# Performance work log

Hardware: AMD Instinct MI355X
Metric: run time of the kernel (lower is better)

Reference implementation:

```python
import jax, jax.numpy as jnp
import numpy as np

K = 8          # max_output_degree (complete 8-ary tree)
DEPTH = 7      # number of levels
LEVEL_OFFS = [(K**l - 1) // (K - 1) for l in range(DEPTH + 1)]  # [0,1,9,73,...]
N = LEVEL_OFFS[DEPTH]  # 299593 nodes
V, X, H, O = 32000, 128, 128, 128


def setup_inputs() -> dict:
    key = jax.random.key(0)
    ks = jax.random.split(key, 7)
    x = jax.random.randint(ks[0], (N,), 0, V, dtype=jnp.int32)
    mask = jnp.ones((N,), dtype=jnp.int32)
    # children of node i are K*i+1 .. K*i+K; out-of-range -> sentinel N (zero pad row)
    ch = np.arange(N, dtype=np.int64)[:, None] * K + 1 + np.arange(K, dtype=np.int64)[None, :]
    children = jnp.asarray(np.where(ch < N, ch, N).astype(np.int32))
    s = 0.02
    emb = jax.random.normal(ks[1], (V, X), dtype=jnp.float32) * s
    W_in = jax.random.normal(ks[2], (X, H), dtype=jnp.float32) * s
    b_in = jnp.zeros((H,), dtype=jnp.float32)
    U = jax.random.normal(ks[3], (H, H), dtype=jnp.float32) * s
    W_out = jax.random.normal(ks[4], (H, O), dtype=jnp.float32) * s
    b_out = jnp.zeros((O,), dtype=jnp.float32)
    return {"x": x, "mask": mask, "children": children, "emb": emb,
            "W_in": W_in, "b_in": b_in, "U": U, "W_out": W_out, "b_out": b_out}


def reference(x, mask, children, emb, W_in, b_in, U, b_out=None, W_out=None, **_):
    # keyword-safe wrapper not used; real signature below
    raise NotImplementedError


def reference(x, mask, children, emb, W_in, b_in, U, W_out, b_out):
    mf = mask.astype(jnp.float32)[:, None]                 # [N,1]
    embeds = emb[x * mask]                                 # [N,X] input_module(x*mask)
    h_input = (embeds @ W_in + b_in) * mf                  # [N,H] W_in(embeds)*mask
    h = jnp.zeros((N + 1, h_input.shape[1]), dtype=h_input.dtype)  # row N = zero pad
    # bottom-up topological propagation, level by level
    for l in range(DEPTH - 1, -1, -1):
        s, e = LEVEL_OFFS[l], LEVEL_OFFS[l + 1]
        if l == DEPTH - 1:
            # leaves: no children messages
            h_new = jnp.tanh(h_input[s:e])
        else:
            h_ch = h[children[s:e]]                        # [n_l,K,H] gather child states
            agg = h_ch.sum(axis=1) @ U                     # SumChild aggregator + linear
            h_new = jnp.tanh(h_input[s:e] + agg)           # apply_node_func
        h = h.at[s:e].set(h_new)
    out = h[:N] @ W_out + b_out                            # output_module
    return out
```

## Files before the change

### kernel.cpp

```cpp
#include <hip/hip_runtime.h>
#include <hip/hip_bf16.h>


typedef __bf16 bf16x8 __attribute__((ext_vector_type(8)));
typedef float f32x4 __attribute__((ext_vector_type(4)));
typedef float f32x2 __attribute__((ext_vector_type(2)));
typedef unsigned short ushort8 __attribute__((ext_vector_type(8)));

#define NNODES 299593

static __device__ __forceinline__ unsigned short f2bf(float f) {
  union { float f; unsigned int u; } v; v.f = f;
  unsigned int u = v.u;
  u += 0x7fff + ((u >> 16) & 1);
  return (unsigned short)(u >> 16);
}

static __device__ __forceinline__ unsigned int pk2bf(float a, float b) {
#if __has_builtin(__builtin_amdgcn_cvt_pk_bf16_f32)
  typedef __bf16 bf16x2 __attribute__((ext_vector_type(2)));
  union { bf16x2 v; unsigned int u; } c;
  c.v = __builtin_amdgcn_cvt_pk_bf16_f32(a, b);
  return c.u;
#else
  return (unsigned int)f2bf(a) | ((unsigned int)f2bf(b) << 16);
#endif
}

static __device__ __forceinline__ float fast_tanh(float x) {
  float y = x * 2.885390081777927f;
#if __has_builtin(__builtin_amdgcn_exp2f)
  float e = __builtin_amdgcn_exp2f(y);
#else
  float e = __builtin_exp2f(y);
#endif
#if __has_builtin(__builtin_amdgcn_rcpf)
  float r = __builtin_amdgcn_rcpf(e + 1.0f);
#else
  float r = 1.0f / (e + 1.0f);
#endif
  return __builtin_fmaf(-2.0f, r, 1.0f);
}

__global__ void prep_weights(const float* __restrict__ W_in,
                             const float* __restrict__ U,
                             const float* __restrict__ W_out,
                             unsigned short* __restrict__ w_sw) {
  int f = blockIdx.x * 256 + threadIdx.x;
  int m = f >> 14;
  int r = f & 16383;
  int j = r & 7;
  int lane = (r >> 3) & 63;
  int nt = (r >> 9) & 7;
  int kt = (r >> 12) & 3;
  int k = kt * 32 + ((lane >> 4) * 8) + j;
  int n = nt * 16 + (lane & 15);
  const float* W = (m == 0) ? W_in : (m == 1) ? U : W_out;
  w_sw[f] = f2bf(W[k * 128 + n]);
}

static __device__ __forceinline__ void gemm16(f32x4 acc[8],
    const unsigned short* a_base, const unsigned short* b_sw, int lane) {
  const int coll = lane & 15;
  const int quad = lane >> 4;
#pragma unroll
  for (int kt = 0; kt < 4; ++kt) {
    bf16x8 a = *(const bf16x8*)(a_base + coll * 136 + kt * 32 + quad * 8);
#pragma unroll
    for (int nt = 0; nt < 8; ++nt) {
      bf16x8 b = *(const bf16x8*)(b_sw + (((kt * 8 + nt) * 64 + lane) * 8));
      acc[nt] = __builtin_amdgcn_mfma_f32_16x16x32_bf16(a, b, acc[nt], 0, 0, 0);
    }
  }
}

template <bool LEAF>
static __device__ __forceinline__ void tile_body(
    const int* __restrict__ x, const int* __restrict__ mask,
    const float* __restrict__ emb, const float* __restrict__ b_in,
    const float* __restrict__ b_out, const unsigned short* __restrict__ w_sw,
    unsigned short* __restrict__ h, float* __restrict__ out,
    int e, int row0, unsigned short (*Abuf)[136], int tid) {
  const int lane = tid & 63;
  const int wave = tid >> 6;

  {
    const int r = tid >> 2;
    const int cg = tid & 3;
    const int grow = row0 + r;
    const int valid = (grow < e);
    const int m = valid ? mask[grow] : 0;
    const int idx = valid ? x[grow] * m : 0;
    const float fm = (float)m;
    const float* erow = emb + (size_t)idx * 128 + cg * 32;
#pragma unroll
    for (int b = 0; b < 4; ++b) {
      f32x4 v0 = *(const f32x4*)(erow + b * 8);
      f32x4 v1 = *(const f32x4*)(erow + b * 8 + 4);
      union { ushort8 s; unsigned int u[4]; } w;
      w.u[0] = pk2bf(v0[0] * fm, v0[1] * fm);
      w.u[1] = pk2bf(v0[2] * fm, v0[3] * fm);
      w.u[2] = pk2bf(v1[0] * fm, v1[1] * fm);
      w.u[3] = pk2bf(v1[2] * fm, v1[3] * fm);
      *(ushort8*)&Abuf[r][cg * 32 + b * 8] = w.s;
    }
  }
  __builtin_amdgcn_wave_barrier();

  f32x4 acc[8];
#pragma unroll
  for (int nt = 0; nt < 8; ++nt) acc[nt] = (f32x4){0.f, 0.f, 0.f, 0.f};
  gemm16(acc, &Abuf[wave * 16][0], w_sw, lane);

  if (!LEAF) {
    const int r = tid >> 2;
    const int cg = tid & 3;
    const int grow = row0 + r;
    f32x2 sums[16];
#pragma unroll
    for (int q = 0; q < 16; ++q) sums[q] = (f32x2){0.f, 0.f};
    if (grow < e) {
      const unsigned short* hp = h + ((size_t)grow * 8 + 1) * 128 + cg * 32;
#pragma unroll
      for (int j = 0; j < 8; ++j) {
#pragma unroll
        for (int b = 0; b < 2; ++b) {
          union { ushort8 s; unsigned int u[4]; } hv;
          hv.s = *(const ushort8*)(hp + j * 128 + b * 16);
#pragma unroll
          for (int q = 0; q < 4; ++q) {
            union { unsigned int u; float f; } lo, hi;
            lo.u = hv.u[q] << 16;
            hi.u = hv.u[q] & 0xffff0000u;
            sums[b * 8 + q] += (f32x2){lo.f, hi.f};
          }
          hv.s = *(const ushort8*)(hp + j * 128 + b * 16 + 8);
#pragma unroll
          for (int q = 0; q < 4; ++q) {
            union { unsigned int u; float f; } lo, hi;
            lo.u = hv.u[q] << 16;
            hi.u = hv.u[q] & 0xffff0000u;
            sums[b * 8 + 4 + q] += (f32x2){lo.f, hi.f};
          }
        }
      }
    }
#pragma unroll
    for (int b = 0; b < 2; ++b) {
      union { ushort8 s; unsigned int u[4]; } w0, w1;
#pragma unroll
      for (int q = 0; q < 4; ++q) {
        w0.u[q] = pk2bf(sums[b * 8 + q][0], sums[b * 8 + q][1]);
        w1.u[q] = pk2bf(sums[b * 8 + 4 + q][0], sums[b * 8 + 4 + q][1]);
      }
      *(ushort8*)&Abuf[r][cg * 32 + b * 16] = w0.s;
      *(ushort8*)&Abuf[r][cg * 32 + b * 16 + 8] = w1.s;
    }
    __builtin_amdgcn_wave_barrier();
    gemm16(acc, &Abuf[wave * 16][0], w_sw + 16384, lane);
  }

  const int coll = lane & 15;
  const int quad = lane >> 4;
  float binv[8];
#pragma unroll
  for (int nt = 0; nt < 8; ++nt) binv[nt] = b_in[nt * 16 + coll];
#pragma unroll
  for (int r2 = 0; r2 < 4; ++r2) {
    const int rowl = wave * 16 + quad * 4 + r2;
    const int grow = row0 + rowl;
    const float mval = (grow < e) ? (float)mask[grow] : 0.f;
#pragma unroll
    for (int nt = 0; nt < 8; ++nt) {
      float t = acc[nt][r2] + mval * binv[nt];
      Abuf[rowl][nt * 16 + coll] = f2bf(fast_tanh(t));
    }
  }
  __builtin_amdgcn_wave_barrier();

  {
    const int sr = wave * 16 + (lane >> 2);
    const int sc = (lane & 3) * 8;
    const int grow = row0 + sr;
    if (grow < e) {
      unsigned short* hp = h + (size_t)grow * 128;
#pragma unroll
      for (int i = 0; i < 4; ++i)
        *(ushort8*)(hp + sc + i * 32) = *(const ushort8*)&Abuf[sr][sc + i * 32];
    }
  }

  f32x4 oacc[8];
#pragma unroll
  for (int nt = 0; nt < 8; ++nt) oacc[nt] = (f32x4){0.f, 0.f, 0.f, 0.f};
  gemm16(oacc, &Abuf[wave * 16][0], w_sw + 32768, lane);

  float boutv[8];
#pragma unroll
  for (int nt = 0; nt < 8; ++nt) boutv[nt] = b_out[nt * 16 + coll];
#pragma unroll
  for (int r2 = 0; r2 < 4; ++r2) {
    const int rowl = wave * 16 + quad * 4 + r2;
    const int grow = row0 + rowl;
    if (grow < e) {
#pragma unroll
      for (int nt = 0; nt < 8; ++nt)
        out[(size_t)grow * 128 + nt * 16 + coll] = oacc[nt][r2] + boutv[nt];
    }
  }
}

template <bool LEAF>
__global__ __launch_bounds__(256) void level_kernel(
    const int* __restrict__ x, const int* __restrict__ mask,
    const float* __restrict__ emb, const float* __restrict__ b_in,
    const float* __restrict__ b_out, const unsigned short* __restrict__ w_sw,
    unsigned short* __restrict__ h, float* __restrict__ out, int s, int e) {
  __shared__ __align__(16) unsigned short Abuf[64][136];
  tile_body<LEAF>(x, mask, emb, b_in, b_out, w_sw, h, out, e,
                  s + blockIdx.x * 64, Abuf, threadIdx.x);
}

__global__ __launch_bounds__(256) void tail_kernel(
    const int* __restrict__ x, const int* __restrict__ mask,
    const float* __restrict__ emb, const float* __restrict__ b_in,
    const float* __restrict__ b_out, const unsigned short* __restrict__ w_sw,
    unsigned short* __restrict__ h, float* __restrict__ out) {
  __shared__ __align__(16) unsigned short Abuf[64][136];
  tile_body<false>(x, mask, emb, b_in, b_out, w_sw, h, out, 73, 9, Abuf,
                   threadIdx.x);
  __syncthreads();
  tile_body<false>(x, mask, emb, b_in, b_out, w_sw, h, out, 9, 1, Abuf,
                   threadIdx.x);
  __syncthreads();
  tile_body<false>(x, mask, emb, b_in, b_out, w_sw, h, out, 1, 0, Abuf,
                   threadIdx.x);
}

extern "C" void kernel_launch(void* const* d_in, const int* in_sizes, int n_in,
                              void* d_out, int out_size, void* d_ws,
                              size_t ws_size, hipStream_t stream) {
  const int* x = (const int*)d_in[0];
  const int* mask = (const int*)d_in[1];
  const float* emb = (const float*)d_in[3];
  const float* W_in = (const float*)d_in[4];
  const float* b_in = (const float*)d_in[5];
  const float* U = (const float*)d_in[6];
  const float* W_out = (const float*)d_in[7];
  const float* b_out = (const float*)d_in[8];
  float* out = (float*)d_out;

  unsigned short* h = (unsigned short*)d_ws;
  unsigned short* w_sw = h + (size_t)NNODES * 128;

  prep_weights<<<192, 256, 0, stream>>>(W_in, U, W_out, w_sw);

  level_kernel<true><<<4096, 256, 0, stream>>>(x, mask, emb, b_in, b_out, w_sw,
                                               h, out, 37449, 299593);
  level_kernel<false><<<512, 256, 0, stream>>>(x, mask, emb, b_in, b_out, w_sw,
                                               h, out, 4681, 37449);
  level_kernel<false><<<64, 256, 0, stream>>>(x, mask, emb, b_in, b_out, w_sw,
                                              h, out, 585, 4681);
  level_kernel<false><<<8, 256, 0, stream>>>(x, mask, emb, b_in, b_out, w_sw,
                                             h, out, 73, 585);
  tail_kernel<<<1, 256, 0, stream>>>(x, mask, emb, b_in, b_out, w_sw, h, out);
}
```

Measured before the change: 316.5 us.

## Precompute child sums in producer level and load bf16 embeddings directly into MFMA

Each level kernel now sums its own 8 sibling rows in shared memory and writes one bf16 child-sum row per parent. The next level reads a single row instead of gathering 8 child h rows, and the full h array is no longer stored. The embedding table is converted to bf16 once in the prep kernel, and A operands are loaded straight from global memory into MFMA registers, skipping the LDS staging. This cuts h write and gather traffic and embedding bytes. In exchange it adds a 32000x128 conversion pass and relies on children being aligned in groups of 8 within tiles.

Result: faster. 278.0 us (-12.2%).

```diff
diff --git a/kernel.cpp b/kernel.cpp
--- a/kernel.cpp
+++ b/kernel.cpp
@@ -6,8 +6,10 @@
 typedef float f32x4 __attribute__((ext_vector_type(4)));
 typedef float f32x2 __attribute__((ext_vector_type(2)));
 typedef unsigned short ushort8 __attribute__((ext_vector_type(8)));
+typedef unsigned int uint2v __attribute__((ext_vector_type(2)));
 
 #define NNODES 299593
+#define NPAR   37449
 
 static __device__ __forceinline__ unsigned short f2bf(float f) {
   union { float f; unsigned int u; } v; v.f = f;
@@ -42,126 +44,100 @@
   return __builtin_fmaf(-2.0f, r, 1.0f);
 }
 
-__global__ void prep_weights(const float* __restrict__ W_in,
-                             const float* __restrict__ U,
-                             const float* __restrict__ W_out,
-                             unsigned short* __restrict__ w_sw) {
-  int f = blockIdx.x * 256 + threadIdx.x;
-  int m = f >> 14;
-  int r = f & 16383;
-  int j = r & 7;
-  int lane = (r >> 3) & 63;
-  int nt = (r >> 9) & 7;
-  int kt = (r >> 12) & 3;
-  int k = kt * 32 + ((lane >> 4) * 8) + j;
-  int n = nt * 16 + (lane & 15);
-  const float* W = (m == 0) ? W_in : (m == 1) ? U : W_out;
-  w_sw[f] = f2bf(W[k * 128 + n]);
-}
-
-static __device__ __forceinline__ void gemm16(f32x4 acc[8],
-    const unsigned short* a_base, const unsigned short* b_sw, int lane) {
-  const int coll = lane & 15;
-  const int quad = lane >> 4;
-#pragma unroll
-  for (int kt = 0; kt < 4; ++kt) {
-    bf16x8 a = *(const bf16x8*)(a_base + coll * 136 + kt * 32 + quad * 8);
-#pragma unroll
-    for (int nt = 0; nt < 8; ++nt) {
-      bf16x8 b = *(const bf16x8*)(b_sw + (((kt * 8 + nt) * 64 + lane) * 8));
-      acc[nt] = __builtin_amdgcn_mfma_f32_16x16x32_bf16(a, b, acc[nt], 0, 0, 0);
-    }
+__global__ __launch_bounds__(256) void prep_kernel(
+    const float* __restrict__ W_in, const float* __restrict__ U,
+    const float* __restrict__ W_out, const float* __restrict__ emb,
+    unsigned short* __restrict__ w_sw, unsigned short* __restrict__ emb_bf) {
+  int t = blockIdx.x * 256 + threadIdx.x;
+  if (blockIdx.x < 192) {
+    int f = t;
+    int m = f >> 14;
+    int r = f & 16383;
+    int j = r & 7;
+    int lane = (r >> 3) & 63;
+    int nt = (r >> 9) & 7;
+    int kt = (r >> 12) & 3;
+    int k = kt * 32 + ((lane >> 4) * 8) + j;
+    int n = nt * 16 + (lane & 15);
+    const float* W = (m == 0) ? W_in : (m == 1) ? U : W_out;
+    w_sw[f] = f2bf(W[k * 128 + n]);
+  } else {
+    size_t i = (size_t)(t - 49152) * 8;
+    f32x4 v0 = *(const f32x4*)(emb + i);
+    f32x4 v1 = *(const f32x4*)(emb + i + 4);
+    union { ushort8 s; unsigned int u[4]; } w;
+    w.u[0] = pk2bf(v0[0], v0[1]);
+    w.u[1] = pk2bf(v0[2], v0[3]);
+    w.u[2] = pk2bf(v1[0], v1[1]);
+    w.u[3] = pk2bf(v1[2], v1[3]);
+    *(ushort8*)(emb_bf + i) = w.s;
+  }
+}
+
+static __device__ __forceinline__ bf16x8 ldz(const unsigned short* p, int nz) {
+  union { bf16x8 b; unsigned int u[4]; } v;
+  v.b = *(const bf16x8*)p;
+  if (!nz) { v.u[0] = 0; v.u[1] = 0; v.u[2] = 0; v.u[3] = 0; }
+  return v.b;
+}
+
+static __device__ __forceinline__ void mfma_row8(f32x4 acc[8], bf16x8 a,
+    const unsigned short* __restrict__ bkt, int lane) {
+#pragma unroll
+  for (int nt = 0; nt < 8; ++nt) {
+    bf16x8 b = *(const bf16x8*)(bkt + nt * 512 + lane * 8);
+    acc[nt] = __builtin_amdgcn_mfma_f32_16x16x32_bf16(a, b, acc[nt], 0, 0, 0);
   }
 }
 
 template <bool LEAF>
 static __device__ __forceinline__ void tile_body(
     const int* __restrict__ x, const int* __restrict__ mask,
-    const float* __restrict__ emb, const float* __restrict__ b_in,
-    const float* __restrict__ b_out, const unsigned short* __restrict__ w_sw,
-    unsigned short* __restrict__ h, float* __restrict__ out,
+    const unsigned short* __restrict__ emb_bf,
+    const float* __restrict__ b_in, const float* __restrict__ b_out,
+    const unsigned short* __restrict__ w_sw,
+    unsigned short* __restrict__ cs, float* __restrict__ out,
     int e, int row0, unsigned short (*Abuf)[136], int tid) {
   const int lane = tid & 63;
   const int wave = tid >> 6;
-
-  {
-    const int r = tid >> 2;
-    const int cg = tid & 3;
-    const int grow = row0 + r;
-    const int valid = (grow < e);
-    const int m = valid ? mask[grow] : 0;
-    const int idx = valid ? x[grow] * m : 0;
-    const float fm = (float)m;
-    const float* erow = emb + (size_t)idx * 128 + cg * 32;
-#pragma unroll
-    for (int b = 0; b < 4; ++b) {
-      f32x4 v0 = *(const f32x4*)(erow + b * 8);
-      f32x4 v1 = *(const f32x4*)(erow + b * 8 + 4);
-      union { ushort8 s; unsigned int u[4]; } w;
-      w.u[0] = pk2bf(v0[0] * fm, v0[1] * fm);
-      w.u[1] = pk2bf(v0[2] * fm, v0[3] * fm);
-      w.u[2] = pk2bf(v1[0] * fm, v1[1] * fm);
-      w.u[3] = pk2bf(v1[2] * fm, v1[3] * fm);
-      *(ushort8*)&Abuf[r][cg * 32 + b * 8] = w.s;
-    }
-  }
-  __builtin_amdgcn_wave_barrier();
-
-  f32x4 acc[8];
-#pragma unroll
-  for (int nt = 0; nt < 8; ++nt) acc[nt] = (f32x4){0.f, 0.f, 0.f, 0.f};
-  gemm16(acc, &Abuf[wave * 16][0], w_sw, lane);
-
-  if (!LEAF) {
-    const int r = tid >> 2;
-    const int cg = tid & 3;
-    const int grow = row0 + r;
-    f32x2 sums[16];
-#pragma unroll
-    for (int q = 0; q < 16; ++q) sums[q] = (f32x2){0.f, 0.f};
-    if (grow < e) {
-      const unsigned short* hp = h + ((size_t)grow * 8 + 1) * 128 + cg * 32;
-#pragma unroll
-      for (int j = 0; j < 8; ++j) {
-#pragma unroll
-        for (int b = 0; b < 2; ++b) {
-          union { ushort8 s; unsigned int u[4]; } hv;
-          hv.s = *(const ushort8*)(hp + j * 128 + b * 16);
-#pragma unroll
-          for (int q = 0; q < 4; ++q) {
-            union { unsigned int u; float f; } lo, hi;
-            lo.u = hv.u[q] << 16;
-            hi.u = hv.u[q] & 0xffff0000u;
-            sums[b * 8 + q] += (f32x2){lo.f, hi.f};
-          }
-          hv.s = *(const ushort8*)(hp + j * 128 + b * 16 + 8);
-#pragma unroll
-          for (int q = 0; q < 4; ++q) {
-            union { unsigned int u; float f; } lo, hi;
-            lo.u = hv.u[q] << 16;
-            hi.u = hv.u[q] & 0xffff0000u;
-            sums[b * 8 + 4 + q] += (f32x2){lo.f, hi.f};
-          }
-        }
-      }
-    }
-#pragma unroll
-    for (int b = 0; b < 2; ++b) {
-      union { ushort8 s; unsigned int u[4]; } w0, w1;
-#pragma unroll
-      for (int q = 0; q < 4; ++q) {
-        w0.u[q] = pk2bf(sums[b * 8 + q][0], sums[b * 8 + q][1]);
-        w1.u[q] = pk2bf(sums[b * 8 + 4 + q][0], sums[b * 8 + 4 + q][1]);
-      }
-      *(ushort8*)&Abuf[r][cg * 32 + b * 16] = w0.s;
-      *(ushort8*)&Abuf[r][cg * 32 + b * 16 + 8] = w1.s;
-    }
-    __builtin_amdgcn_wave_barrier();
-    gemm16(acc, &Abuf[wave * 16][0], w_sw + 16384, lane);
-  }
-
   const int coll = lane & 15;
   const int quad = lane >> 4;
+
+  const int garow = row0 + wave * 16 + coll;
+  const int valid = garow < e;
+  const int m = valid ? mask[garow] : 0;
+  const int idx = valid ? x[garow] * m : 0;
+
+  const unsigned short* arow = emb_bf + (size_t)idx * 128 + quad * 8;
+  bf16x8 ea0 = ldz(arow, m);
+  bf16x8 ea1 = ldz(arow + 32, m);
+  bf16x8 ea2 = ldz(arow + 64, m);
+  bf16x8 ea3 = ldz(arow + 96, m);
+  bf16x8 ca0, ca1, ca2, ca3;
+  if (!LEAF) {
+    const unsigned short* crow = cs + (size_t)garow * 128 + quad * 8;
+    ca0 = ldz(crow, valid);
+    ca1 = ldz(crow + 32, valid);
+    ca2 = ldz(crow + 64, valid);
+    ca3 = ldz(crow + 96, valid);
+  }
+
+  f32x4 acc[8];
+#pragma unroll
+  for (int nt = 0; nt < 8; ++nt) acc[nt] = (f32x4){0.f, 0.f, 0.f, 0.f};
+
+  mfma_row8(acc, ea0, w_sw, lane);
+  mfma_row8(acc, ea1, w_sw + 4096, lane);
+  mfma_row8(acc, ea2, w_sw + 8192, lane);
+  mfma_row8(acc, ea3, w_sw + 12288, lane);
+
+  if (!LEAF) {
+    mfma_row8(acc, ca0, w_sw + 16384, lane);
+    mfma_row8(acc, ca1, w_sw + 20480, lane);
+    mfma_row8(acc, ca2, w_sw + 24576, lane);
+    mfma_row8(acc, ca3, w_sw + 28672, lane);
+  }
+
   float binv[8];
 #pragma unroll
   for (int nt = 0; nt < 8; ++nt) binv[nt] = b_in[nt * 16 + coll];
@@ -178,22 +154,41 @@
   }
   __builtin_amdgcn_wave_barrier();
 
-  {
-    const int sr = wave * 16 + (lane >> 2);
-    const int sc = (lane & 3) * 8;
-    const int grow = row0 + sr;
-    if (grow < e) {
-      unsigned short* hp = h + (size_t)grow * 128;
-#pragma unroll
-      for (int i = 0; i < 4; ++i)
-        *(ushort8*)(hp + sc + i * 32) = *(const ushort8*)&Abuf[sr][sc + i * 32];
+  if (row0 > 0) {
+    const int j = lane >> 5;
+    const int c4 = (lane & 31) * 4;
+    const int childrow0 = row0 + (wave * 2 + j) * 8;
+    if (childrow0 < e) {
+      const int lr0 = wave * 16 + j * 8;
+      f32x2 sA = {0.f, 0.f}, sB = {0.f, 0.f};
+#pragma unroll
+      for (int r = 0; r < 8; ++r) {
+        const unsigned int* pr =
+            (const unsigned int*)&Abuf[lr0 + r][c4];
+        unsigned int u0 = pr[0], u1 = pr[1];
+        union { unsigned int u; float f; } l0, h0, l1, h1;
+        l0.u = u0 << 16; h0.u = u0 & 0xffff0000u;
+        l1.u = u1 << 16; h1.u = u1 & 0xffff0000u;
+        sA += (f32x2){l0.f, h0.f};
+        sB += (f32x2){l1.f, h1.f};
+      }
+      uint2v w;
+      w.x = pk2bf(sA[0], sA[1]);
+      w.y = pk2bf(sB[0], sB[1]);
+      const int p = ((row0 - 1) >> 3) + wave * 2 + j;
+      *(uint2v*)(cs + (size_t)p * 128 + c4) = w;
     }
   }
 
   f32x4 oacc[8];
 #pragma unroll
   for (int nt = 0; nt < 8; ++nt) oacc[nt] = (f32x4){0.f, 0.f, 0.f, 0.f};
-  gemm16(oacc, &Abuf[wave * 16][0], w_sw + 32768, lane);
+  const unsigned short* ab = &Abuf[wave * 16][0] + coll * 136 + quad * 8;
+#pragma unroll
+  for (int kt = 0; kt < 4; ++kt) {
+    bf16x8 a = *(const bf16x8*)(ab + kt * 32);
+    mfma_row8(oacc, a, w_sw + 32768 + kt * 4096, lane);
+  }
 
   float boutv[8];
 #pragma unroll
@@ -213,27 +208,27 @@
 template <bool LEAF>
 __global__ __launch_bounds__(256) void level_kernel(
     const int* __restrict__ x, const int* __restrict__ mask,
-    const float* __restrict__ emb, const float* __restrict__ b_in,
+    const unsigned short* __restrict__ emb_bf, const float* __restrict__ b_in,
     const float* __restrict__ b_out, const unsigned short* __restrict__ w_sw,
-    unsigned short* __restrict__ h, float* __restrict__ out, int s, int e) {
+    unsigned short* __restrict__ cs, float* __restrict__ out, int s, int e) {
   __shared__ __align__(16) unsigned short Abuf[64][136];
-  tile_body<LEAF>(x, mask, emb, b_in, b_out, w_sw, h, out, e,
+  tile_body<LEAF>(x, mask, emb_bf, b_in, b_out, w_sw, cs, out, e,
                   s + blockIdx.x * 64, Abuf, threadIdx.x);
 }
 
 __global__ __launch_bounds__(256) void tail_kernel(
     const int* __restrict__ x, const int* __restrict__ mask,
-    const float* __restrict__ emb, const float* __restrict__ b_in,
+    const unsigned short* __restrict__ emb_bf, const float* __restrict__ b_in,
     const float* __restrict__ b_out, const unsigned short* __restrict__ w_sw,
-    unsigned short* __restrict__ h, float* __restrict__ out) {
+    unsigned short* __restrict__ cs, float* __restrict__ out) {
   __shared__ __align__(16) unsigned short Abuf[64][136];
-  tile_body<false>(x, mask, emb, b_in, b_out, w_sw, h, out, 73, 9, Abuf,
+  tile_body<false>(x, mask, emb_bf, b_in, b_out, w_sw, cs, out, 73, 9, Abuf,
                    threadIdx.x);
   __syncthreads();
-  tile_body<false>(x, mask, emb, b_in, b_out, w_sw, h, out, 9, 1, Abuf,
+  tile_body<false>(x, mask, emb_bf, b_in, b_out, w_sw, cs, out, 9, 1, Abuf,
                    threadIdx.x);
   __syncthreads();
-  tile_body<false>(x, mask, emb, b_in, b_out, w_sw, h, out, 1, 0, Abuf,
+  tile_body<false>(x, mask, emb_bf, b_in, b_out, w_sw, cs, out, 1, 0, Abuf,
                    threadIdx.x);
 }
 
@@ -250,18 +245,20 @@
   const float* b_out = (const float*)d_in[8];
   float* out = (float*)d_out;
 
-  unsigned short* h = (unsigned short*)d_ws;
-  unsigned short* w_sw = h + (size_t)NNODES * 128;
-
-  prep_weights<<<192, 256, 0, stream>>>(W_in, U, W_out, w_sw);
-
-  level_kernel<true><<<4096, 256, 0, stream>>>(x, mask, emb, b_in, b_out, w_sw,
-                                               h, out, 37449, 299593);
-  level_kernel<false><<<512, 256, 0, stream>>>(x, mask, emb, b_in, b_out, w_sw,
-                                               h, out, 4681, 37449);
-  level_kernel<false><<<64, 256, 0, stream>>>(x, mask, emb, b_in, b_out, w_sw,
-                                              h, out, 585, 4681);
-  level_kernel<false><<<8, 256, 0, stream>>>(x, mask, emb, b_in, b_out, w_sw,
-                                             h, out, 73, 585);
-  tail_kernel<<<1, 256, 0, stream>>>(x, mask, emb, b_in, b_out, w_sw, h, out);
-}
+  unsigned short* emb_bf = (unsigned short*)d_ws;
+  unsigned short* cs = emb_bf + (size_t)32000 * 128;
+  unsigned short* w_sw = cs + (size_t)NPAR * 128;
+
+  prep_kernel<<<2192, 256, 0, stream>>>(W_in, U, W_out, emb, w_sw, emb_bf);
+
+  level_kernel<true><<<4096, 256, 0, stream>>>(x, mask, emb_bf, b_in, b_out,
+                                               w_sw, cs, out, 37449, 299593);
+  level_kernel<false><<<512, 256, 0, stream>>>(x, mask, emb_bf, b_in, b_out,
+                                               w_sw, cs, out, 4681, 37449);
+  level_kernel<false><<<64, 256, 0, stream>>>(x, mask, emb_bf, b_in, b_out,
+                                              w_sw, cs, out, 585, 4681);
+  level_kernel<false><<<8, 256, 0, stream>>>(x, mask, emb_bf, b_in, b_out,
+                                             w_sw, cs, out, 73, 585);
+  tail_kernel<<<1, 256, 0, stream>>>(x, mask, emb_bf, b_in, b_out, w_sw, cs,
+                                     out);
+}
```
